# Kernel tuning notes

Measured on AMD Instinct MI355X. Metric: run time of the kernel, lower is better.

The kernel has to match this reference:

```python
import jax, jax.numpy as jnp
import numpy as np

B, S, M, E, DFF = 4, 2048, 1024, 8, 4096
CAPACITY_FACTOR = 1.25


def setup_inputs() -> dict:
    key = jax.random.key(0)
    k = jax.random.split(key, 5)
    x = jax.random.normal(k[0], (B, S, M), dtype=jnp.float32)
    wg = jax.random.normal(k[1], (M, E), dtype=jnp.float32) * 0.02
    w1 = jax.random.normal(k[2], (E, M, DFF), dtype=jnp.float32) * 0.02
    b1 = jnp.zeros((E, DFF), dtype=jnp.float32)
    w2 = jax.random.normal(k[3], (E, DFF, M), dtype=jnp.float32) * 0.02
    b2 = jnp.zeros((E, M), dtype=jnp.float32)
    return {"x": x, "wg": wg, "w1": w1, "b1": b1, "w2": w2, "b2": b2}


def _top1_gate(tokens, wg, capacity):
    # tokens: [T, M] -> combine_weights [T, E, C], dispatch_mask [T, E, C]
    gates = jax.nn.softmax(tokens @ wg)                      # [T, E]
    expert_idx = jnp.argmax(gates, axis=-1)                  # [T]
    mask1 = jax.nn.one_hot(expert_idx, gates.shape[-1], dtype=gates.dtype)  # [T, E]
    # position of each token within its chosen expert's queue
    pos = jnp.sum(jnp.cumsum(mask1, axis=0) * mask1, axis=-1).astype(jnp.int32) - 1  # [T]
    keep = (pos < capacity).astype(gates.dtype)              # capacity drop
    mask1c = mask1 * keep[:, None]                           # [T, E]
    gates1 = jnp.sum(gates * mask1c, axis=-1)                # chosen prob (0 if dropped)
    loc_oh = jax.nn.one_hot(pos, capacity, dtype=gates.dtype)  # [T, C] (>=C rows -> all 0)
    combine = gates1[:, None, None] * mask1c[:, :, None] * loc_oh[:, None, :]  # [T, E, C]
    dispatch = (combine > 0).astype(tokens.dtype)
    return combine, dispatch


def reference(x, wg, w1, b1, w2, b2):
    d_model = x.shape[-1]
    tokens = x.reshape(-1, d_model)                          # [T, M]
    T = tokens.shape[0]
    num_experts = wg.shape[1]
    capacity = int(CAPACITY_FACTOR * T / num_experts)        # C
    combine, dispatch = _top1_gate(tokens, wg, capacity)
    # dispatch tokens to per-expert buffers: [E, C, M]
    dispatched = jnp.einsum('sec,sm->ecm', dispatch, tokens)
    # per-expert FFN (batched over experts)
    h = jax.nn.relu(jnp.einsum('ecm,emf->ecf', dispatched, w1) + b1[:, None, :])
    expert_out = jnp.einsum('ecf,efm->ecm', h, w2) + b2[:, None, :]
    # combine back to tokens
    combined = jnp.einsum('sec,ecm->sm', combine, expert_out)
    return combined.reshape(x.shape)
```

## Files before the change

### kernel.cpp

```cpp
#include <hip/hip_runtime.h>

#define T_TOKENS 8192
#define MDIM 1024
#define NEXP 8
#define DFF_DIM 4096
#define CAP 1280

typedef __attribute__((ext_vector_type(8))) short short8;
typedef __attribute__((ext_vector_type(4))) float f32x4;

__device__ inline unsigned short f2bf(float f) {
  unsigned u = __float_as_uint(f);
  u = u + 0x7fffu + ((u >> 16) & 1u);
  return (unsigned short)(u >> 16);
}

__global__ __launch_bounds__(64) void gate_kernel(const float* __restrict__ x,
    const float* __restrict__ wg, int* __restrict__ eidx, float* __restrict__ gate)
{
  const int t = blockIdx.x;
  const int lane = threadIdx.x;
  const float* xr = x + (size_t)t * MDIM;
  double acc[NEXP];
  #pragma unroll
  for (int e = 0; e < NEXP; ++e) acc[e] = 0.0;
  for (int m = lane; m < MDIM; m += 64) {
    double xv = (double)xr[m];
    const float* wr = wg + (size_t)m * NEXP;
    #pragma unroll
    for (int e = 0; e < NEXP; ++e) acc[e] += xv * (double)wr[e];
  }
  #pragma unroll
  for (int off = 32; off > 0; off >>= 1) {
    #pragma unroll
    for (int e = 0; e < NEXP; ++e) acc[e] += __shfl_down(acc[e], off);
  }
  if (lane == 0) {
    double mx = acc[0]; int idx = 0;
    #pragma unroll
    for (int e = 1; e < NEXP; ++e) if (acc[e] > mx) { mx = acc[e]; idx = e; }
    double s = 0.0;
    #pragma unroll
    for (int e = 0; e < NEXP; ++e) s += exp(acc[e] - mx);
    eidx[t] = idx;
    gate[t] = (float)(1.0 / s);
  }
}

__global__ __launch_bounds__(1024) void scan_kernel(const int* __restrict__ eidx,
    int* __restrict__ slot_token, int* __restrict__ filled)
{
  __shared__ int hist[16][NEXP];
  __shared__ int wpre[16][NEXP];
  __shared__ int rtot[NEXP];
  __shared__ int base[NEXP];
  const int tid = threadIdx.x;
  const int w = tid >> 6, lane = tid & 63;
  for (int i = tid; i < NEXP * CAP; i += 1024) slot_token[i] = -1;
  if (tid < NEXP) base[tid] = 0;
  __syncthreads();
  const unsigned long long lt = (1ull << lane) - 1ull;
  for (int r = 0; r < T_TOKENS / 1024; ++r) {
    const int t = r * 1024 + tid;
    const int e = eidx[t];
    unsigned long long bal[NEXP];
    #pragma unroll
    for (int ee = 0; ee < NEXP; ++ee) bal[ee] = __ballot(e == ee);
    const int rank = __popcll(bal[e] & lt);
    if (lane < NEXP) hist[w][lane] = __popcll(bal[lane]);
    __syncthreads();
    if (tid < 16 * NEXP) {
      int ww = tid >> 3, ee = tid & 7, s = 0;
      for (int j = 0; j < ww; ++j) s += hist[j][ee];
      wpre[ww][ee] = s;
    }
    if (tid < NEXP) {
      int s = 0;
      for (int j = 0; j < 16; ++j) s += hist[j][tid];
      rtot[tid] = s;
    }
    __syncthreads();
    const int pos = base[e] + wpre[w][e] + rank;
    if (pos < CAP) slot_token[e * CAP + pos] = t;
    __syncthreads();
    if (tid < NEXP) base[tid] += rtot[tid];
    __syncthreads();
  }
  if (tid < NEXP) filled[tid] = (base[tid] < CAP) ? base[tid] : CAP;
}

__global__ __launch_bounds__(256) void dispatch_kernel(const float* __restrict__ x,
    const int* __restrict__ slot_token, unsigned short* __restrict__ Abuf)
{
  const int row = blockIdx.x;
  const int tid = threadIdx.x;
  const int t = slot_token[row];
  unsigned short* dst = Abuf + (size_t)row * MDIM + tid * 4;
  if (t < 0) {
    ushort4 z; z.x = 0; z.y = 0; z.z = 0; z.w = 0;
    *(ushort4*)dst = z;
  } else {
    const float4 v = *(const float4*)(x + (size_t)t * MDIM + tid * 4);
    ushort4 h;
    h.x = f2bf(v.x); h.y = f2bf(v.y); h.z = f2bf(v.z); h.w = f2bf(v.w);
    *(ushort4*)dst = h;
  }
}

template<int MODE>
__global__ __launch_bounds__(256) void gemm_kernel(
    const unsigned short* __restrict__ A, const float* __restrict__ Bw,
    const float* __restrict__ bias, void* __restrict__ outp,
    const int* __restrict__ slot_token, const float* __restrict__ gate,
    const int* __restrict__ filled)
{
  constexpr int N = MODE ? MDIM : DFF_DIM;
  constexpr int K = MODE ? DFF_DIM : MDIM;
  const int e = blockIdx.z;
  const int rowbase = blockIdx.y * 128;
  const int colbase = blockIdx.x * 128;
  if (rowbase >= filled[e]) return;

  __shared__ unsigned short As[128][40];
  __shared__ unsigned short Bs[128][40];

  const int tid = threadIdx.x;
  const int lane = tid & 63;
  const int wid = tid >> 6;
  const int wm = (wid >> 1) * 64, wn = (wid & 1) * 64;
  const int qm = lane & 15, qk = (lane >> 4) * 8, qr = lane >> 4;

  const unsigned short* Ab = A + ((size_t)e * CAP + rowbase) * K;
  const float* Bb = Bw + (size_t)e * K * N + colbase;

  f32x4 acc[4][4];
  #pragma unroll
  for (int i = 0; i < 4; ++i)
    #pragma unroll
    for (int j = 0; j < 4; ++j)
      #pragma unroll
      for (int r = 0; r < 4; ++r) acc[i][j][r] = 0.0f;

  for (int k0 = 0; k0 < K; k0 += 32) {
    __syncthreads();
    #pragma unroll
    for (int i = 0; i < 2; ++i) {
      const int c = tid + i * 256;
      const int m = c >> 2, kq = c & 3;
      const uint4 v = *(const uint4*)(Ab + (size_t)m * K + k0 + kq * 8);
      *(uint4*)&As[m][kq * 8] = v;
    }
    #pragma unroll
    for (int i = 0; i < 4; ++i) {
      const int c = tid + i * 256;
      const int n = c & 127, kq = c >> 7;
      const float* bp = Bb + (size_t)(k0 + kq * 4) * N + n;
      ushort4 h;
      h.x = f2bf(bp[0]);
      h.y = f2bf(bp[(size_t)N]);
      h.z = f2bf(bp[(size_t)2 * N]);
      h.w = f2bf(bp[(size_t)3 * N]);
      *(ushort4*)&Bs[n][kq * 4] = h;
    }
    __syncthreads();
    short8 af[4], bfr[4];
    #pragma unroll
    for (int i = 0; i < 4; ++i) af[i] = *(const short8*)&As[wm + i * 16 + qm][qk];
    #pragma unroll
    for (int j = 0; j < 4; ++j) bfr[j] = *(const short8*)&Bs[wn + j * 16 + qm][qk];
    #pragma unroll
    for (int i = 0; i < 4; ++i)
      #pragma unroll
      for (int j = 0; j < 4; ++j)
        acc[i][j] = __builtin_amdgcn_mfma_f32_16x16x32_bf16(af[i], bfr[j], acc[i][j], 0, 0, 0);
  }

  float bcol[4];
  #pragma unroll
  for (int j = 0; j < 4; ++j)
    bcol[j] = bias[(size_t)e * N + colbase + wn + j * 16 + qm];

  if (MODE == 0) {
    unsigned short* Hp = (unsigned short*)outp;
    #pragma unroll
    for (int i = 0; i < 4; ++i) {
      #pragma unroll
      for (int r = 0; r < 4; ++r) {
        const int row = rowbase + wm + i * 16 + qr * 4 + r;
        unsigned short* orow = Hp + ((size_t)e * CAP + row) * N + colbase;
        #pragma unroll
        for (int j = 0; j < 4; ++j) {
          float v = acc[i][j][r] + bcol[j];
          v = v > 0.0f ? v : 0.0f;
          orow[wn + j * 16 + qm] = f2bf(v);
        }
      }
    }
  } else {
    float* Op = (float*)outp;
    #pragma unroll
    for (int i = 0; i < 4; ++i) {
      #pragma unroll
      for (int r = 0; r < 4; ++r) {
        const int row = rowbase + wm + i * 16 + qr * 4 + r;
        const int t = slot_token[e * CAP + row];
        if (t >= 0) {
          const float g = gate[t];
          float* orow = Op + (size_t)t * MDIM + colbase;
          #pragma unroll
          for (int j = 0; j < 4; ++j)
            orow[wn + j * 16 + qm] = g * (acc[i][j][r] + bcol[j]);
        }
      }
    }
  }
}

extern "C" void kernel_launch(void* const* d_in, const int* in_sizes, int n_in,
                              void* d_out, int out_size, void* d_ws, size_t ws_size,
                              hipStream_t stream) {
  const float* x  = (const float*)d_in[0];
  const float* wg = (const float*)d_in[1];
  const float* w1 = (const float*)d_in[2];
  const float* b1 = (const float*)d_in[3];
  const float* w2 = (const float*)d_in[4];
  const float* b2 = (const float*)d_in[5];

  char* ws = (char*)d_ws;
  unsigned short* Abuf = (unsigned short*)ws;
  unsigned short* H    = (unsigned short*)(ws + 20971520);
  int*   slot_token    = (int*)(ws + 104857600);
  int*   eidx          = (int*)(ws + 104898560);
  float* gate          = (float*)(ws + 104931328);
  int*   filled        = (int*)(ws + 104964096);

  hipMemsetAsync(d_out, 0, (size_t)out_size * sizeof(float), stream);

  gate_kernel<<<T_TOKENS, 64, 0, stream>>>(x, wg, eidx, gate);
  scan_kernel<<<1, 1024, 0, stream>>>(eidx, slot_token, filled);
  dispatch_kernel<<<NEXP * CAP, 256, 0, stream>>>(x, slot_token, Abuf);

  dim3 g1(DFF_DIM / 128, CAP / 128, NEXP);
  gemm_kernel<0><<<g1, 256, 0, stream>>>(Abuf, w1, b1, (void*)H, nullptr, nullptr, filled);

  dim3 g2(MDIM / 128, CAP / 128, NEXP);
  gemm_kernel<1><<<g2, 256, 0, stream>>>(H, w2, b2, d_out, slot_token, gate, filled);
}
```

Measured before the change: 623.2 us.

## Pre-transpose weights to bf16 and stage GEMM tiles with async global-to-LDS loads

Adds a transpose-and-convert kernel that turns each expert's fp32 W1 and W2 into bf16, K-contiguous layout in workspace before its GEMM. The GEMM then fills its shared-memory tiles with 16-byte global_load_lds transfers instead of per-element fp32 loads plus bf16 conversion in every block. This removes conversion work that was repeated across row-blocks and halves the weight bytes read inside the GEMM. In exchange it adds two extra passes over the full weight tensors. The LDS tiles also lose their padding, which can cause bank conflicts on fragment reads.

```diff
diff --git a/kernel.cpp b/kernel.cpp
--- a/kernel.cpp
+++ b/kernel.cpp
@@ -13,6 +13,12 @@
   unsigned u = __float_as_uint(f);
   u = u + 0x7fffu + ((u >> 16) & 1u);
   return (unsigned short)(u >> 16);
+}
+
+__device__ __forceinline__ void async_ld16(const void* g, void* l) {
+  __builtin_amdgcn_global_load_lds(
+      (__attribute__((address_space(1))) void*)const_cast<void*>(g),
+      (__attribute__((address_space(3))) void*)l, 16, 0, 0);
 }
 
 __global__ __launch_bounds__(64) void gate_kernel(const float* __restrict__ x,
@@ -107,9 +113,44 @@
   }
 }
 
+template<int R, int Cc>
+__global__ __launch_bounds__(256) void transpose_cvt_kernel(
+    const float* __restrict__ src, unsigned short* __restrict__ dst)
+{
+  __shared__ unsigned short tile[64][66];
+  const int e = blockIdx.z;
+  const int r0 = blockIdx.y * 64;
+  const int c0 = blockIdx.x * 64;
+  const int t = threadIdx.x;
+  const float* S = src + (size_t)e * R * Cc;
+  unsigned short* D = dst + (size_t)e * R * Cc;
+  const int tr = t >> 4;
+  const int tc = (t & 15) * 4;
+  #pragma unroll
+  for (int i = 0; i < 4; ++i) {
+    const int row = i * 16 + tr;
+    const float4 v = *(const float4*)(S + (size_t)(r0 + row) * Cc + c0 + tc);
+    tile[row][tc + 0] = f2bf(v.x);
+    tile[row][tc + 1] = f2bf(v.y);
+    tile[row][tc + 2] = f2bf(v.z);
+    tile[row][tc + 3] = f2bf(v.w);
+  }
+  __syncthreads();
+  #pragma unroll
+  for (int i = 0; i < 4; ++i) {
+    const int crow = i * 16 + tr;
+    ushort4 o;
+    o.x = tile[tc + 0][crow];
+    o.y = tile[tc + 1][crow];
+    o.z = tile[tc + 2][crow];
+    o.w = tile[tc + 3][crow];
+    *(ushort4*)(D + (size_t)(c0 + crow) * R + r0 + tc) = o;
+  }
+}
+
 template<int MODE>
 __global__ __launch_bounds__(256) void gemm_kernel(
-    const unsigned short* __restrict__ A, const float* __restrict__ Bw,
+    const unsigned short* __restrict__ A, const unsigned short* __restrict__ Bt,
     const float* __restrict__ bias, void* __restrict__ outp,
     const int* __restrict__ slot_token, const float* __restrict__ gate,
     const int* __restrict__ filled)
@@ -121,8 +162,8 @@
   const int colbase = blockIdx.x * 128;
   if (rowbase >= filled[e]) return;
 
-  __shared__ unsigned short As[128][40];
-  __shared__ unsigned short Bs[128][40];
+  __shared__ unsigned short As[128 * 32];
+  __shared__ unsigned short Bs[128 * 32];
 
   const int tid = threadIdx.x;
   const int lane = tid & 63;
@@ -131,7 +172,14 @@
   const int qm = lane & 15, qk = (lane >> 4) * 8, qr = lane >> 4;
 
   const unsigned short* Ab = A + ((size_t)e * CAP + rowbase) * K;
-  const float* Bb = Bw + (size_t)e * K * N + colbase;
+  const unsigned short* Bb = Bt + ((size_t)e * N + colbase) * K;
+
+  const int ldr = wid * 16 + (lane >> 2);
+  const int ldk = (lane & 3) * 8;
+  const unsigned short* ag = Ab + (size_t)ldr * K + ldk;
+  const unsigned short* bg = Bb + (size_t)ldr * K + ldk;
+  unsigned short* asw = As + wid * 512;
+  unsigned short* bsw = Bs + wid * 512;
 
   f32x4 acc[4][4];
   #pragma unroll
@@ -143,31 +191,16 @@
 
   for (int k0 = 0; k0 < K; k0 += 32) {
     __syncthreads();
-    #pragma unroll
-    for (int i = 0; i < 2; ++i) {
-      const int c = tid + i * 256;
-      const int m = c >> 2, kq = c & 3;
-      const uint4 v = *(const uint4*)(Ab + (size_t)m * K + k0 + kq * 8);
-      *(uint4*)&As[m][kq * 8] = v;
-    }
-    #pragma unroll
-    for (int i = 0; i < 4; ++i) {
-      const int c = tid + i * 256;
-      const int n = c & 127, kq = c >> 7;
-      const float* bp = Bb + (size_t)(k0 + kq * 4) * N + n;
-      ushort4 h;
-      h.x = f2bf(bp[0]);
-      h.y = f2bf(bp[(size_t)N]);
-      h.z = f2bf(bp[(size_t)2 * N]);
-      h.w = f2bf(bp[(size_t)3 * N]);
-      *(ushort4*)&Bs[n][kq * 4] = h;
-    }
+    async_ld16(ag + k0,                asw);
+    async_ld16(ag + (size_t)64 * K + k0, asw + 2048);
+    async_ld16(bg + k0,                bsw);
+    async_ld16(bg + (size_t)64 * K + k0, bsw + 2048);
     __syncthreads();
     short8 af[4], bfr[4];
     #pragma unroll
-    for (int i = 0; i < 4; ++i) af[i] = *(const short8*)&As[wm + i * 16 + qm][qk];
-    #pragma unroll
-    for (int j = 0; j < 4; ++j) bfr[j] = *(const short8*)&Bs[wn + j * 16 + qm][qk];
+    for (int i = 0; i < 4; ++i) af[i] = *(const short8*)(As + (wm + i * 16 + qm) * 32 + qk);
+    #pragma unroll
+    for (int j = 0; j < 4; ++j) bfr[j] = *(const short8*)(Bs + (wn + j * 16 + qm) * 32 + qk);
     #pragma unroll
     for (int i = 0; i < 4; ++i)
       #pragma unroll
@@ -229,10 +262,11 @@
   char* ws = (char*)d_ws;
   unsigned short* Abuf = (unsigned short*)ws;
   unsigned short* H    = (unsigned short*)(ws + 20971520);
-  int*   slot_token    = (int*)(ws + 104857600);
-  int*   eidx          = (int*)(ws + 104898560);
-  float* gate          = (float*)(ws + 104931328);
-  int*   filled        = (int*)(ws + 104964096);
+  unsigned short* Wt   = (unsigned short*)(ws + 104857600);
+  int*   slot_token    = (int*)(ws + 171966464);
+  int*   eidx          = (int*)(ws + 172007424);
+  float* gate          = (float*)(ws + 172040192);
+  int*   filled        = (int*)(ws + 172072960);
 
   hipMemsetAsync(d_out, 0, (size_t)out_size * sizeof(float), stream);
 
@@ -240,9 +274,15 @@
   scan_kernel<<<1, 1024, 0, stream>>>(eidx, slot_token, filled);
   dispatch_kernel<<<NEXP * CAP, 256, 0, stream>>>(x, slot_token, Abuf);
 
+  dim3 gc1(DFF_DIM / 64, MDIM / 64, NEXP);
+  transpose_cvt_kernel<MDIM, DFF_DIM><<<gc1, 256, 0, stream>>>(w1, Wt);
+
   dim3 g1(DFF_DIM / 128, CAP / 128, NEXP);
-  gemm_kernel<0><<<g1, 256, 0, stream>>>(Abuf, w1, b1, (void*)H, nullptr, nullptr, filled);
+  gemm_kernel<0><<<g1, 256, 0, stream>>>(Abuf, Wt, b1, (void*)H, nullptr, nullptr, filled);
+
+  dim3 gc2(MDIM / 64, DFF_DIM / 64, NEXP);
+  transpose_cvt_kernel<DFF_DIM, MDIM><<<gc2, 256, 0, stream>>>(w2, Wt);
 
   dim3 g2(MDIM / 128, CAP / 128, NEXP);
-  gemm_kernel<1><<<g2, 256, 0, stream>>>(H, w2, b2, d_out, slot_token, gate, filled);
-}
+  gemm_kernel<1><<<g2, 256, 0, stream>>>(H, Wt, b2, d_out, slot_token, gate, filled);
+}
```

Measured after the change: 581.8 us. -6.6%, faster.
